# Optimization experiments

Hardware: AMD Instinct MI355X
Metric: run time of the kernel (lower is better)

The kernel has to match this reference:

```python
import jax, jax.numpy as jnp
import numpy as np

B, Q, K, D = 8, 2048, 2048, 512

def setup_inputs() -> dict:
    key = jax.random.key(0)
    k1, k2, k3, k4, k5 = jax.random.split(key, 5)
    return {
        "query": jax.random.normal(k1, (B, Q, D), dtype=jnp.float32),
        "key": jax.random.normal(k2, (B, K, D), dtype=jnp.float32),
        "value": jax.random.normal(k3, (B, K, D), dtype=jnp.float32),
        "key_mask": jax.random.randint(k4, (B, K), 0, 2, dtype=jnp.int32),
        "W": jax.random.normal(k5, (D, D), dtype=jnp.float32) / np.sqrt(D),
    }

def reference(query, key, value, key_mask, W):
    # bilinear score: s[b,q,k] = query[b,q,:] @ W @ key[b,k,:]
    scale = 1.0 / jnp.sqrt(jnp.asarray(query.shape[-1], query.dtype))
    qW = jnp.einsum('bqd,de->bqe', query, W)          # [B,Q,D]
    scores = jnp.einsum('bqe,bke->bqk', qW, key)      # [B,Q,K]
    scores = jnp.where(key_mask[:, None, :] == 0, jnp.asarray(-1e20, scores.dtype), scores) * scale
    dist = jax.nn.softmax(scores, axis=-1)            # [B,Q,K]
    context = jnp.einsum('bqk,bkd->bqd', dist, value) # [B,Q,D]
    return context, dist
```

## Files before the change

### kernel.cpp

```cpp
#include <hip/hip_runtime.h>
#include <stdint.h>

#define BB 8
#define QQ 2048
#define KK 2048
#define DD 512

typedef _Float16 f16x8 __attribute__((ext_vector_type(8)));
typedef float f32x4 __attribute__((ext_vector_type(4)));

__device__ __forceinline__ unsigned short f2h(float f) {
    union { _Float16 h; unsigned short u; } x;
    x.h = (_Float16)f;
    return x.u;
}
__device__ __forceinline__ float h2f(unsigned short u) {
    union { unsigned short u; _Float16 h; } x;
    x.u = u;
    return (float)x.h;
}

__device__ __forceinline__ void async16(const unsigned short* g, unsigned short* l) {
    __builtin_amdgcn_global_load_lds(
        (const __attribute__((address_space(1))) unsigned int*)g,
        (__attribute__((address_space(3))) unsigned int*)l, 16, 0, 0);
}

__global__ __launch_bounds__(256) void cvt_f32_f16(const float* __restrict__ in,
                                                   unsigned short* __restrict__ out) {
    size_t i = ((size_t)blockIdx.x * 256 + threadIdx.x) * 8;
    float4 a = *(const float4*)(in + i);
    float4 b = *(const float4*)(in + i + 4);
    uint4 u;
    u.x = (unsigned)f2h(a.x) | ((unsigned)f2h(a.y) << 16);
    u.y = (unsigned)f2h(a.z) | ((unsigned)f2h(a.w) << 16);
    u.z = (unsigned)f2h(b.x) | ((unsigned)f2h(b.y) << 16);
    u.w = (unsigned)f2h(b.z) | ((unsigned)f2h(b.w) << 16);
    *(uint4*)(out + i) = u;
}

__global__ __launch_bounds__(256) void transpose_cvt(const float* __restrict__ in,
                                                     unsigned short* __restrict__ out,
                                                     int R, int C, long inB, long outB) {
    __shared__ float t[32][33];
    const float* ip = in + (size_t)blockIdx.z * inB;
    unsigned short* op = out + (size_t)blockIdx.z * outB;
    int x = threadIdx.x & 31, y0 = threadIdx.x >> 5;
    int c0 = blockIdx.x * 32, r0 = blockIdx.y * 32;
#pragma unroll
    for (int i = 0; i < 32; i += 8)
        t[y0 + i][x] = ip[(size_t)(r0 + y0 + i) * C + c0 + x];
    __syncthreads();
#pragma unroll
    for (int i = 0; i < 32; i += 8)
        op[(size_t)(c0 + y0 + i) * R + r0 + x] = f2h(t[x][y0 + i]);
}

template <int OUTM>
__global__ __launch_bounds__(256) void gemm_bt(const unsigned short* __restrict__ Aall,
                                               const unsigned short* __restrict__ Ball,
                                               void* __restrict__ Call,
                                               const int* __restrict__ maskAll,
                                               float* __restrict__ sums,
                                               int Kred, int lda, int ldb, int ldc,
                                               long aStride, long bStride, long cStride,
                                               int maskStride, float scale) {
    const int b = blockIdx.z;
    const int m0 = blockIdx.y * 128;
    const int n0 = blockIdx.x * 128;

    __shared__ unsigned short As[128 * 32];
    __shared__ unsigned short Bs[128 * 32];

    const int tid = threadIdx.x;
    const int lane = tid & 63, wave = tid >> 6;
    const int wm = wave >> 1, wn = wave & 1;
    const int lrow = lane & 15, quad = lane >> 4;

    const int ar = tid >> 2, ac = (tid & 3) * 8;

    const unsigned short* Ab = Aall + (size_t)b * aStride + (size_t)m0 * lda;
    const unsigned short* Bb = Ball + (size_t)b * bStride + (size_t)n0 * ldb;
    unsigned short* AsW = As + wave * 512;
    unsigned short* BsW = Bs + wave * 512;

    f32x4 acc[4][4];
#pragma unroll
    for (int mi = 0; mi < 4; mi++)
#pragma unroll
        for (int ni = 0; ni < 4; ni++)
            acc[mi][ni] = (f32x4){0.f, 0.f, 0.f, 0.f};

    for (int kk = 0; kk < Kred; kk += 32) {
#pragma unroll
        for (int j = 0; j < 2; j++)
            async16(Ab + (size_t)(j * 64 + ar) * lda + kk + ac, AsW + j * 2048);
#pragma unroll
        for (int j = 0; j < 2; j++)
            async16(Bb + (size_t)(j * 64 + ar) * ldb + kk + ac, BsW + j * 2048);
        __syncthreads();

        f16x8 af[4], bfr[4];
#pragma unroll
        for (int i = 0; i < 4; i++)
            af[i] = *(const f16x8*)&As[(wm * 64 + i * 16 + lrow) * 32 + quad * 8];
#pragma unroll
        for (int i = 0; i < 4; i++)
            bfr[i] = *(const f16x8*)&Bs[(wn * 64 + i * 16 + lrow) * 32 + quad * 8];

#pragma unroll
        for (int mi = 0; mi < 4; mi++)
#pragma unroll
            for (int ni = 0; ni < 4; ni++)
                acc[mi][ni] = __builtin_amdgcn_mfma_f32_16x16x32_f16(af[mi], bfr[ni],
                                                                     acc[mi][ni], 0, 0, 0);
        __syncthreads();
    }

#pragma unroll
    for (int mi = 0; mi < 4; mi++) {
        const int gm = m0 + wm * 64 + mi * 16 + quad * 4;
        if constexpr (OUTM == 0) {
            unsigned short* C = (unsigned short*)Call + (size_t)b * cStride;
#pragma unroll
            for (int ni = 0; ni < 4; ni++) {
                int gn = n0 + wn * 64 + ni * 16 + lrow;
#pragma unroll
                for (int r = 0; r < 4; r++)
                    C[(size_t)(gm + r) * ldc + gn] = f2h(acc[mi][ni][r]);
            }
        } else if constexpr (OUTM == 1) {
            unsigned short* C = (unsigned short*)Call + (size_t)b * cStride;
            const int* mk = maskAll + (size_t)b * maskStride;
            float ps[4] = {0.f, 0.f, 0.f, 0.f};
#pragma unroll
            for (int ni = 0; ni < 4; ni++) {
                int gn = n0 + wn * 64 + ni * 16 + lrow;
                bool keep = mk[gn] != 0;
#pragma unroll
                for (int r = 0; r < 4; r++) {
                    float e = keep ? __expf(acc[mi][ni][r] * scale) : 0.f;
                    C[(size_t)(gm + r) * ldc + gn] = f2h(e);
                    ps[r] += e;
                }
            }
#pragma unroll
            for (int off = 1; off < 16; off <<= 1)
#pragma unroll
                for (int r = 0; r < 4; r++) ps[r] += __shfl_xor(ps[r], off);
            if (lrow == 0) {
                float* s = sums + (size_t)b * QQ;
#pragma unroll
                for (int r = 0; r < 4; r++) atomicAdd(&s[gm + r], ps[r]);
            }
        } else {
            float* C = (float*)Call + (size_t)b * cStride;
            const float* s = sums + (size_t)b * QQ;
            float iv[4];
#pragma unroll
            for (int r = 0; r < 4; r++) iv[r] = 1.0f / s[gm + r];
#pragma unroll
            for (int ni = 0; ni < 4; ni++) {
                int gn = n0 + wn * 64 + ni * 16 + lrow;
#pragma unroll
                for (int r = 0; r < 4; r++)
                    C[(size_t)(gm + r) * ldc + gn] = acc[mi][ni][r] * iv[r];
            }
        }
    }
}

__global__ __launch_bounds__(256) void normalize_rows(const unsigned short* __restrict__ expS,
                                                      const float* __restrict__ sums,
                                                      float* __restrict__ dist) {
    const unsigned short* sp = expS + (size_t)blockIdx.x * 2048;
    float* dp = dist + (size_t)blockIdx.x * 2048;
    const float inv = 1.0f / sums[blockIdx.x];
    int tid = threadIdx.x;

    uint4 u = *(const uint4*)(sp + tid * 8);
    float4 o0, o1;
    o0.x = h2f((unsigned short)(u.x & 0xffff)) * inv;
    o0.y = h2f((unsigned short)(u.x >> 16)) * inv;
    o0.z = h2f((unsigned short)(u.y & 0xffff)) * inv;
    o0.w = h2f((unsigned short)(u.y >> 16)) * inv;
    o1.x = h2f((unsigned short)(u.z & 0xffff)) * inv;
    o1.y = h2f((unsigned short)(u.z >> 16)) * inv;
    o1.z = h2f((unsigned short)(u.w & 0xffff)) * inv;
    o1.w = h2f((unsigned short)(u.w >> 16)) * inv;
    *(float4*)(dp + tid * 8) = o0;
    *(float4*)(dp + tid * 8 + 4) = o1;
}

extern "C" void kernel_launch(void* const* d_in, const int* in_sizes, int n_in,
                              void* d_out, int out_size, void* d_ws, size_t ws_size,
                              hipStream_t stream) {
    const float* q    = (const float*)d_in[0];
    const float* k    = (const float*)d_in[1];
    const float* v    = (const float*)d_in[2];
    const int*   mask = (const int*)d_in[3];
    const float* W    = (const float*)d_in[4];

    float* ctx  = (float*)d_out;
    float* dist = ctx + (size_t)BB * QQ * DD;

    unsigned short* ws  = (unsigned short*)d_ws;
    unsigned short* Wt  = ws;
    unsigned short* Qh  = Wt + (size_t)DD * DD;
    unsigned short* Kh  = Qh + (size_t)BB * QQ * DD;
    unsigned short* Vt  = Kh + (size_t)BB * KK * DD;
    unsigned short* qWh = Vt + (size_t)BB * DD * KK;
    unsigned short* Sc  = qWh + (size_t)BB * QQ * DD;
    float* sums = (float*)(Sc + (size_t)BB * QQ * KK);

    const float scale = 0.044194173824159216f;

    hipMemsetAsync(sums, 0, (size_t)BB * QQ * sizeof(float), stream);
    transpose_cvt<<<dim3(DD / 32, DD / 32, 1), 256, 0, stream>>>(W, Wt, DD, DD, 0, 0);
    cvt_f32_f16<<<dim3((BB * QQ * DD / 8) / 256), 256, 0, stream>>>(q, Qh);
    cvt_f32_f16<<<dim3((BB * KK * DD / 8) / 256), 256, 0, stream>>>(k, Kh);
    transpose_cvt<<<dim3(DD / 32, KK / 32, BB), 256, 0, stream>>>(
        v, Vt, KK, DD, (long)KK * DD, (long)DD * KK);
    gemm_bt<0><<<dim3(DD / 128, QQ / 128, BB), 256, 0, stream>>>(
        Qh, Wt, qWh, nullptr, nullptr, DD, DD, DD, DD,
        (long)QQ * DD, 0, (long)QQ * DD, 0, 0.f);
    gemm_bt<1><<<dim3(KK / 128, QQ / 128, BB), 256, 0, stream>>>(
        qWh, Kh, Sc, mask, sums, DD, DD, DD, KK,
        (long)QQ * DD, (long)KK * DD, (long)QQ * KK, KK, scale);
    normalize_rows<<<dim3(BB * QQ), 256, 0, stream>>>(Sc, sums, dist);
    gemm_bt<2><<<dim3(DD / 128, QQ / 128, BB), 256, 0, stream>>>(
        Sc, Vt, ctx, nullptr, sums, KK, KK, KK, DD,
        (long)QQ * KK, (long)DD * KK, (long)QQ * DD, 0, 0.f);
}
```

Before: 421.8 us.

## Fuse dist normalization into PV GEMM and remap workgroups across XCDs

Removes the separate normalize_rows pass by having the final GEMM write normalized fp32 dist rows straight from the exp-score tiles already staged in LDS. The four column-blocks of each row tile each write a disjoint K range, using nontemporal stores. It also remaps workgroup IDs so that consecutive logical tiles are grouped on the same XCD, which should improve L2 reuse for all GEMMs. The aim is to avoid re-reading the fp16 scores from global memory, at the cost of adding store traffic inside the GEMM's main loop.

```diff
diff --git a/kernel.cpp b/kernel.cpp
--- a/kernel.cpp
+++ b/kernel.cpp
@@ -62,12 +62,22 @@
                                                void* __restrict__ Call,
                                                const int* __restrict__ maskAll,
                                                float* __restrict__ sums,
+                                               float* __restrict__ distOut,
                                                int Kred, int lda, int ldb, int ldc,
                                                long aStride, long bStride, long cStride,
                                                int maskStride, float scale) {
-    const int b = blockIdx.z;
-    const int m0 = blockIdx.y * 128;
-    const int n0 = blockIdx.x * 128;
+    const int gx = gridDim.x, gy = gridDim.y;
+    const int nwg = gx * gy * (int)gridDim.z;
+    const int p = ((int)blockIdx.z * gy + (int)blockIdx.y) * gx + (int)blockIdx.x;
+    const int qch = nwg >> 3, rch = nwg & 7;
+    const int xcd = p & 7, ooff = p >> 3;
+    const int w = (xcd < rch ? xcd * (qch + 1) : rch * (qch + 1) + (xcd - rch) * qch) + ooff;
+    const int b = w / (gx * gy);
+    const int rem = w - b * (gx * gy);
+    const int my = rem / gx;
+    const int nx = rem - my * gx;
+    const int m0 = my * 128;
+    const int n0 = nx * 128;
 
     __shared__ unsigned short As[128 * 32];
     __shared__ unsigned short Bs[128 * 32];
@@ -84,6 +94,20 @@
     unsigned short* AsW = As + wave * 512;
     unsigned short* BsW = Bs + wave * 512;
 
+    float invRow = 0.f;
+    const unsigned short* dsrc = nullptr;
+    float* dp = nullptr;
+    int dklo = 0, dkhi = 0;
+    if constexpr (OUTM == 2) {
+        const int drow = tid >> 1, dcol = (tid & 1) * 16;
+        invRow = 1.0f / sums[(size_t)b * QQ + m0 + drow];
+        dsrc = As + drow * 32 + dcol;
+        dp = distOut + (size_t)b * QQ * KK + (size_t)(m0 + drow) * KK + dcol;
+        const int kper = Kred / gx;
+        dklo = nx * kper;
+        dkhi = dklo + kper;
+    }
+
     f32x4 acc[4][4];
 #pragma unroll
     for (int mi = 0; mi < 4; mi++)
@@ -114,6 +138,23 @@
             for (int ni = 0; ni < 4; ni++)
                 acc[mi][ni] = __builtin_amdgcn_mfma_f32_16x16x32_f16(af[mi], bfr[ni],
                                                                      acc[mi][ni], 0, 0, 0);
+
+        if constexpr (OUTM == 2) {
+            if (kk >= dklo && kk < dkhi) {
+                f16x8 h0 = *(const f16x8*)dsrc;
+                f16x8 h1 = *(const f16x8*)(dsrc + 8);
+                float vals[16];
+#pragma unroll
+                for (int i = 0; i < 8; i++) vals[i] = (float)h0[i] * invRow;
+#pragma unroll
+                for (int i = 0; i < 8; i++) vals[8 + i] = (float)h1[i] * invRow;
+#pragma unroll
+                for (int i = 0; i < 4; i++) {
+                    f32x4 o = {vals[4 * i], vals[4 * i + 1], vals[4 * i + 2], vals[4 * i + 3]};
+                    __builtin_nontemporal_store(o, (f32x4*)(dp + kk + 4 * i));
+                }
+            }
+        }
         __syncthreads();
     }
 
@@ -168,28 +209,6 @@
             }
         }
     }
-}
-
-__global__ __launch_bounds__(256) void normalize_rows(const unsigned short* __restrict__ expS,
-                                                      const float* __restrict__ sums,
-                                                      float* __restrict__ dist) {
-    const unsigned short* sp = expS + (size_t)blockIdx.x * 2048;
-    float* dp = dist + (size_t)blockIdx.x * 2048;
-    const float inv = 1.0f / sums[blockIdx.x];
-    int tid = threadIdx.x;
-
-    uint4 u = *(const uint4*)(sp + tid * 8);
-    float4 o0, o1;
-    o0.x = h2f((unsigned short)(u.x & 0xffff)) * inv;
-    o0.y = h2f((unsigned short)(u.x >> 16)) * inv;
-    o0.z = h2f((unsigned short)(u.y & 0xffff)) * inv;
-    o0.w = h2f((unsigned short)(u.y >> 16)) * inv;
-    o1.x = h2f((unsigned short)(u.z & 0xffff)) * inv;
-    o1.y = h2f((unsigned short)(u.z >> 16)) * inv;
-    o1.z = h2f((unsigned short)(u.w & 0xffff)) * inv;
-    o1.w = h2f((unsigned short)(u.w >> 16)) * inv;
-    *(float4*)(dp + tid * 8) = o0;
-    *(float4*)(dp + tid * 8 + 4) = o1;
 }
 
 extern "C" void kernel_launch(void* const* d_in, const int* in_sizes, int n_in,
@@ -215,20 +234,19 @@
 
     const float scale = 0.044194173824159216f;
 
-    hipMemsetAsync(sums, 0, (size_t)BB * QQ * sizeof(float), stream);
+    (void)hipMemsetAsync(sums, 0, (size_t)BB * QQ * sizeof(float), stream);
     transpose_cvt<<<dim3(DD / 32, DD / 32, 1), 256, 0, stream>>>(W, Wt, DD, DD, 0, 0);
     cvt_f32_f16<<<dim3((BB * QQ * DD / 8) / 256), 256, 0, stream>>>(q, Qh);
     cvt_f32_f16<<<dim3((BB * KK * DD / 8) / 256), 256, 0, stream>>>(k, Kh);
     transpose_cvt<<<dim3(DD / 32, KK / 32, BB), 256, 0, stream>>>(
         v, Vt, KK, DD, (long)KK * DD, (long)DD * KK);
     gemm_bt<0><<<dim3(DD / 128, QQ / 128, BB), 256, 0, stream>>>(
-        Qh, Wt, qWh, nullptr, nullptr, DD, DD, DD, DD,
+        Qh, Wt, qWh, nullptr, nullptr, nullptr, DD, DD, DD, DD,
         (long)QQ * DD, 0, (long)QQ * DD, 0, 0.f);
     gemm_bt<1><<<dim3(KK / 128, QQ / 128, BB), 256, 0, stream>>>(
-        qWh, Kh, Sc, mask, sums, DD, DD, DD, KK,
+        qWh, Kh, Sc, mask, sums, nullptr, DD, DD, DD, KK,
         (long)QQ * DD, (long)KK * DD, (long)QQ * KK, KK, scale);
-    normalize_rows<<<dim3(BB * QQ), 256, 0, stream>>>(Sc, sums, dist);
     gemm_bt<2><<<dim3(DD / 128, QQ / 128, BB), 256, 0, stream>>>(
-        Sc, Vt, ctx, nullptr, sums, KK, KK, KK, DD,
+        Sc, Vt, ctx, nullptr, sums, dist, KK, KK, KK, DD,
         (long)QQ * KK, (long)DD * KK, (long)QQ * DD, 0, 0.f);
 }
```

New measurement: 538.6 us. +27.7%, slower.
